# Kernel optimization log

Measured on AMD Instinct MI355X. Metric: run time of the kernel, lower is better.

## Reference

```python
import jax, jax.numpy as jnp
import numpy as np

HEADS = (4, 2, 1)
OUTS = (32, 16, 2)
NEG_SLOPE = 0.2


def gat_conv(x, src, dst, W, att_s, att_d, b, heads, out_dim, n_nodes, concat):
    # x: [N, Fin] -> h: [N, H, Fout]
    h = (x @ W).reshape(n_nodes, heads, out_dim)
    # per-node attention terms, gathered to edges: [E, H]
    a_src = jnp.sum(h * att_s, axis=-1)
    a_dst = jnp.sum(h * att_d, axis=-1)
    logits = jax.nn.leaky_relu(a_src[src] + a_dst[dst], NEG_SLOPE)
    # segment softmax over incoming edges of each destination node
    lmax = jax.ops.segment_max(logits, dst, num_segments=n_nodes)[dst]
    e = jnp.exp(logits - lmax)
    denom = jax.ops.segment_sum(e, dst, num_segments=n_nodes)[dst]
    alpha = e / denom  # [E, H]
    # weighted message aggregation
    msg = h[src] * alpha[:, :, None]  # [E, H, Fout]
    agg = jax.ops.segment_sum(msg, dst, num_segments=n_nodes)  # [N, H, Fout]
    if concat:
        agg = agg.reshape(n_nodes, heads * out_dim)
    else:
        agg = agg.mean(axis=1)
    return agg + b


def _glorot(key, shape):
    fan = shape[0] + shape[-1] if len(shape) == 2 else shape[-1] * 2
    s = jnp.sqrt(6.0 / fan)
    return jax.random.uniform(key, shape, jnp.float32, -s, s)


def setup_inputs() -> dict:
    key = jax.random.key(0)
    N, E, FIN = 100000, 1600000, 128
    ks = jax.random.split(key, 16)
    x = jax.random.normal(ks[0], (N, FIN), jnp.float32)
    edge_index = jax.random.randint(ks[1], (2, E), 0, N, jnp.int64)
    ins = (FIN, HEADS[0] * OUTS[0], HEADS[1] * OUTS[1])
    d = {"x": x, "edge_index": edge_index}
    for i in range(3):
        H, O = HEADS[i], OUTS[i]
        d[f"W{i+1}"] = _glorot(ks[2 + 4 * i], (ins[i], H * O))
        d[f"att_s{i+1}"] = _glorot(ks[3 + 4 * i], (H, O))
        d[f"att_d{i+1}"] = _glorot(ks[4 + 4 * i], (H, O))
        bdim = H * O if i < 2 else O
        d[f"b{i+1}"] = jnp.zeros((bdim,), jnp.float32)
    return d


def reference(x, edge_index, W1, att_s1, att_d1, b1, W2, att_s2, att_d2, b2, W3, att_s3, att_d3, b3):
    N = x.shape[0]
    loops = jnp.arange(N, dtype=edge_index.dtype)
    src = jnp.concatenate([edge_index[0], loops])
    dst = jnp.concatenate([edge_index[1], loops])
    h = gat_conv(x, src, dst, W1, att_s1, att_d1, b1, HEADS[0], OUTS[0], N, True)
    h = jax.nn.elu(h)
    h = gat_conv(h, src, dst, W2, att_s2, att_d2, b2, HEADS[1], OUTS[1], N, True)
    h = jax.nn.elu(h)
    h = gat_conv(h, src, dst, W3, att_s3, att_d3, b3, HEADS[2], OUTS[2], N, False)
    return jax.nn.log_softmax(h, axis=1)
```

## Files before the change

kernel.cpp:

```cpp
#include <hip/hip_runtime.h>
#include <math.h>

static __device__ __forceinline__ float lrelu(float x){ return fmaxf(x, 0.2f*x); }
static __device__ __forceinline__ float eluf(float x){ return x > 0.f ? x : __expf(x)-1.f; }
static __device__ __forceinline__ unsigned short f2bf(float f){
  unsigned int u = __float_as_uint(f);
  unsigned int r = (u + 0x7FFFu + ((u>>16)&1u)) >> 16;
  return (unsigned short)r;
}
static __device__ __forceinline__ float bflo(unsigned int u){ return __uint_as_float(u<<16); }
static __device__ __forceinline__ float bfhi(unsigned int u){ return __uint_as_float(u & 0xFFFF0000u); }

typedef __attribute__((ext_vector_type(8))) short short8;
typedef __attribute__((ext_vector_type(4))) float f32x4;

#define DETECT_IS64(ei_, s_is64_) \
  if (threadIdx.x < 64){ \
    int w_ = ((const int*)(ei_))[2*threadIdx.x + 1]; \
    unsigned long long b_ = __ballot(w_ != 0); \
    if (threadIdx.x == 0) s_is64_ = (b_ == 0ull); \
  } \
  __syncthreads();

__global__ void k_wprep(const float* __restrict__ W1, const float* __restrict__ W2,
                        unsigned short* __restrict__ wf1, unsigned short* __restrict__ wf2,
                        int* __restrict__ gbcnt, int* __restrict__ done, int NB){
  int e = blockIdx.x*256 + threadIdx.x;
  if (e < NB) gbcnt[e] = 0;
  if (e == 0) *done = 0;
  if (e < 2048){
    int lane = e&63, ct = (e>>6)&7, ks = e>>9;
    int q = lane>>4, n = lane&15;
    union { unsigned short us[8]; uint4 u; } pk;
    #pragma unroll
    for (int j=0;j<8;j++)
      pk.us[j] = f2bf(W1[(ks*32 + q*8 + j)*128 + ct*16 + n]);
    *(uint4*)&wf1[(size_t)e*8] = pk.u;
  } else if (e < 2048+512){
    int e2 = e - 2048;
    int lane = e2&63, ct = (e2>>6)&1, ks = e2>>7;
    int q = lane>>4, n = lane&15;
    union { unsigned short us[8]; uint4 u; } pk;
    #pragma unroll
    for (int j=0;j<8;j++)
      pk.us[j] = f2bf(W2[(ks*32 + q*8 + j)*32 + ct*16 + n]);
    *(uint4*)&wf2[(size_t)e2*8] = pk.u;
  }
}

__global__ __launch_bounds__(256) void k_bhist_scan(const void* __restrict__ ei,
    int* __restrict__ gbcnt, int* __restrict__ gbbase, int* __restrict__ gcursor,
    int* __restrict__ done, int E, int NB){
  extern __shared__ int lcnt[];
  __shared__ int s_is64;
  __shared__ int s_last;
  __shared__ int sh[256];
  __shared__ int carry;
  int t = threadIdx.x;
  for (int i=t; i<NB; i+=256) lcnt[i]=0;
  DETECT_IS64(ei, s_is64)
  int stride = gridDim.x*256;
  if (s_is64){
    const long long* p = (const long long*)ei;
    for (int e = blockIdx.x*256 + t; e < E; e += stride)
      atomicAdd(&lcnt[((int)p[(size_t)E+e])>>7], 1);
  } else {
    const int* p = (const int*)ei;
    for (int e = blockIdx.x*256 + t; e < E; e += stride)
      atomicAdd(&lcnt[p[(size_t)E+e]>>7], 1);
  }
  __syncthreads();
  for (int i=t; i<NB; i+=256){
    int c = lcnt[i];
    if (c) atomicAdd(&gbcnt[i], c);
  }
  __threadfence();
  if (t == 0){
    int old = atomicAdd(done, 1);
    s_last = (old == (int)gridDim.x - 1) ? 1 : 0;
  }
  __syncthreads();
  if (!s_last) return;
  if (t==0) carry = 0;
  __syncthreads();
  for (int base=0; base<NB; base+=256){
    int idx = base+t;
    int v = (idx<NB) ? atomicAdd(&gbcnt[idx], 0) : 0;
    sh[t]=v; __syncthreads();
    for (int off=1; off<256; off<<=1){
      int add = (t>=off)? sh[t-off] : 0;
      __syncthreads();
      sh[t]+=add;
      __syncthreads();
    }
    int excl = sh[t]-v+carry;
    if (idx<NB){ gbbase[idx]=excl; gcursor[idx]=excl; }
    __syncthreads();
    if (t==0) carry += sh[255];
    __syncthreads();
  }
}

#define BS_ITEMS 16
__global__ __launch_bounds__(256) void k_scat_gemm1(
    const void* __restrict__ ei, int* __restrict__ gcursor,
    unsigned int* __restrict__ ebuf, int E, int NB, int GS,
    const float* __restrict__ x, const unsigned short* __restrict__ wf,
    const float* __restrict__ atts, const float* __restrict__ attd,
    unsigned short* __restrict__ hb, float* __restrict__ as_, float* __restrict__ ad_,
    int N){
  __shared__ __align__(16) unsigned char smem[50176];
  __shared__ int s_is64;
  int t = threadIdx.x;
  if ((int)blockIdx.x < GS){
    int* lcnt  = (int*)smem;
    int* lbase = lcnt + NB;
    for (int i=t; i<NB; i+=256) lcnt[i]=0;
    DETECT_IS64(ei, s_is64)
    bool is64 = s_is64 != 0;
    int base = blockIdx.x*(256*BS_ITEMS);
    unsigned int ent[BS_ITEMS]; int bk[BS_ITEMS];
    #pragma unroll
    for (int i=0;i<BS_ITEMS;i++){
      int e = base + i*256 + t;
      if (e < E){
        int s, d;
        if (is64){ const long long* p=(const long long*)ei; s=(int)p[e]; d=(int)p[(size_t)E+e]; }
        else     { const int* p=(const int*)ei;            s=p[e];      d=p[(size_t)E+e]; }
        int b = d>>7;
        bk[i] = b;
        ent[i] = (unsigned int)s | ((unsigned int)(d & 127) << 25);
        atomicAdd(&lcnt[b], 1);
      } else bk[i] = -1;
    }
    __syncthreads();
    for (int i=t; i<NB; i+=256){
      int c = lcnt[i];
      lbase[i] = c ? atomicAdd(&gcursor[i], c) : 0;
    }
    __syncthreads();
    for (int i=t; i<NB; i+=256) lcnt[i]=0;
    __syncthreads();
    #pragma unroll
    for (int i=0;i<BS_ITEMS;i++){
      if (bk[i] >= 0){
        int pos = lbase[bk[i]] + atomicAdd(&lcnt[bk[i]], 1);
        ebuf[pos] = ent[i];
      }
    }
  } else {
    unsigned short* xs  = (unsigned short*)smem;
    unsigned short* wsm = (unsigned short*)(smem + 64*136*2);
    int r0 = ((int)blockIdx.x - GS)*64;
    {
      const uint4* src = (const uint4*)wf;
      uint4* dst = (uint4*)wsm;
      #pragma unroll
      for (int i=0;i<8;i++) dst[t + i*256] = src[t + i*256];
    }
    {
      #pragma unroll
      for (int i=0;i<4;i++){
        int idx = t + i*256;
        int row = idx>>4, k8 = (idx&15)*8;
        int gr = r0 + row;
        float4 v0 = make_float4(0.f,0.f,0.f,0.f), v1 = v0;
        if (gr < N){
          v0 = *(const float4*)&x[(size_t)gr*128 + k8];
          v1 = *(const float4*)&x[(size_t)gr*128 + k8 + 4];
        }
        union { unsigned short us[8]; uint4 u; } pk;
        pk.us[0]=f2bf(v0.x); pk.us[1]=f2bf(v0.y); pk.us[2]=f2bf(v0.z); pk.us[3]=f2bf(v0.w);
        pk.us[4]=f2bf(v1.x); pk.us[5]=f2bf(v1.y); pk.us[6]=f2bf(v1.z); pk.us[7]=f2bf(v1.w);
        *(uint4*)&xs[row*136 + k8] = pk.u;
      }
    }
    __syncthreads();
    int w = t>>6, lane = t&63, lm = lane&15, q = lane>>4;
    int rt0 = (w&1)*2;
    int ct0 = (w>>1)*4;
    f32x4 acc[2][4];
    #pragma unroll
    for (int a=0;a<2;a++)
      #pragma unroll
      for (int c=0;c<4;c++) acc[a][c] = (f32x4){0.f,0.f,0.f,0.f};
    #pragma unroll
    for (int ks=0;ks<4;ks++){
      short8 a0 = *(const short8*)&xs[( rt0   *16 + lm)*136 + ks*32 + q*8];
      short8 a1 = *(const short8*)&xs[((rt0+1)*16 + lm)*136 + ks*32 + q*8];
      #pragma unroll
      for (int c=0;c<4;c++){
        short8 b = *(const short8*)&wsm[((ks*8 + ct0 + c)*64 + lane)*8];
        acc[0][c] = __builtin_amdgcn_mfma_f32_16x16x32_bf16(a0, b, acc[0][c], 0,0,0);
        acc[1][c] = __builtin_amdgcn_mfma_f32_16x16x32_bf16(a1, b, acc[1][c], 0,0,0);
      }
    }
    __syncthreads();
    #pragma unroll
    for (int rl=0;rl<2;rl++)
      #pragma unroll
      for (int c=0;c<4;c++)
        #pragma unroll
        for (int r=0;r<4;r++)
          xs[((rt0+rl)*16 + q*4 + r)*136 + (ct0+c)*16 + lm] = f2bf(acc[rl][c][r]);
    __syncthreads();
    {
      #pragma unroll
      for (int i=0;i<4;i++){
        int idx = t + i*256;
        int row = idx>>4, c8 = (idx&15)*8;
        int gr = r0 + row;
        if (gr < N)
          *(uint4*)&hb[(size_t)gr*128 + c8] = *(const uint4*)&xs[row*136 + c8];
      }
    }
    {
      int row = t>>2, h = t&3;
      int gr = r0 + row;
      if (gr < N){
        const unsigned short* hr = &xs[row*136 + h*32];
        const float* sa = atts + h*32;
        const float* da = attd + h*32;
        float ss = 0.f, dd = 0.f;
        #pragma unroll
        for (int o=0;o<32;o+=8){
          uint4 v = *(const uint4*)&hr[o];
          float hv[8] = { bflo(v.x),bfhi(v.x),bflo(v.y),bfhi(v.y),
                          bflo(v.z),bfhi(v.z),bflo(v.w),bfhi(v.w) };
          #pragma unroll
          for (int m=0;m<8;m++){ ss += hv[m]*sa[o+m]; dd += hv[m]*da[o+m]; }
        }
        as_[gr*4+h] = ss; ad_[gr*4+h] = dd;
      }
    }
  }
}

__global__ __launch_bounds__(256) void k_bcsr(const unsigned int* __restrict__ ebuf,
    const int* __restrict__ gbbase, const int* __restrict__ gbcnt,
    int* __restrict__ rp, int* __restrict__ csr, int N, int NB, int E){
  __shared__ int lcnt[128];
  __shared__ int lexc[128];
  __shared__ int lcur[128];
  __shared__ int sc[256];
  int b = blockIdx.x, t = threadIdx.x;
  int d0 = b<<7;
  int R = N - d0; if (R > 128) R = 128;
  if (t < 128){ lcnt[t]=0; lcur[t]=0; }
  __syncthreads();
  int base = gbbase[b], cnt = gbcnt[b];
  for (int i=t; i<cnt; i+=256){
    unsigned int e = ebuf[base+i];
    atomicAdd(&lcnt[e>>25], 1);
  }
  __syncthreads();
  int v = (t<128)? lcnt[t] : 0;
  sc[t]=v; __syncthreads();
  for (int off=1; off<128; off<<=1){
    int add = (t>=off)? sc[t-off] : 0;
    __syncthreads();
    sc[t]+=add;
    __syncthreads();
  }
  if (t<128) lexc[t] = sc[t]-v;
  __syncthreads();
  if (t < R) rp[d0+t] = base + lexc[t];
  if (b == NB-1 && t == 0) rp[N] = E;
  for (int i=t; i<cnt; i+=256){
    unsigned int e = ebuf[base+i];
    int dl = e>>25;
    int pos = base + lexc[dl] + atomicAdd(&lcur[dl], 1);
    csr[pos] = (int)(e & 0x1FFFFFFu);
  }
}

__global__ __launch_bounds__(256) void k_mgemm2(const unsigned short* __restrict__ xb,
    const unsigned short* __restrict__ wf,
    const float* __restrict__ atts, const float* __restrict__ attd,
    unsigned short* __restrict__ hb2, float* __restrict__ as_, float* __restrict__ ad_,
    int N){
  __shared__ unsigned short xs[128*136];
  __shared__ unsigned short wsm[512*8];
  int t = threadIdx.x;
  int r0 = blockIdx.x*128;
  {
    #pragma unroll
    for (int i=0;i<2;i++)
      ((uint4*)wsm)[t + i*256] = ((const uint4*)wf)[t + i*256];
  }
  {
    #pragma unroll
    for (int i=0;i<8;i++){
      int idx = t + i*256;
      int row = idx>>4, c8 = (idx&15)*8;
      int gr = r0 + row;
      uint4 v = make_uint4(0u,0u,0u,0u);
      if (gr < N) v = *(const uint4*)&xb[(size_t)gr*128 + c8];
      *(uint4*)&xs[row*136 + c8] = v;
    }
  }
  __syncthreads();
  int w = t>>6, lane = t&63, lm = lane&15, q = lane>>4;
  int rt0 = 2*w;
  f32x4 acc[2][2];
  #pragma unroll
  for (int a=0;a<2;a++){ acc[a][0] = (f32x4){0.f,0.f,0.f,0.f}; acc[a][1] = acc[a][0]; }
  #pragma unroll
  for (int ks=0;ks<4;ks++){
    short8 a0 = *(const short8*)&xs[( rt0   *16 + lm)*136 + ks*32 + q*8];
    short8 a1 = *(const short8*)&xs[((rt0+1)*16 + lm)*136 + ks*32 + q*8];
    #pragma unroll
    for (int c=0;c<2;c++){
      short8 b = *(const short8*)&wsm[((ks*2 + c)*64 + lane)*8];
      acc[0][c] = __builtin_amdgcn_mfma_f32_16x16x32_bf16(a0, b, acc[0][c], 0,0,0);
      acc[1][c] = __builtin_amdgcn_mfma_f32_16x16x32_bf16(a1, b, acc[1][c], 0,0,0);
    }
  }
  __syncthreads();
  #pragma unroll
  for (int rl=0;rl<2;rl++)
    #pragma unroll
    for (int c=0;c<2;c++)
      #pragma unroll
      for (int r=0;r<4;r++)
        xs[((rt0+rl)*16 + q*4 + r)*136 + c*16 + lm] = f2bf(acc[rl][c][r]);
  __syncthreads();
  {
    #pragma unroll
    for (int i=0;i<2;i++){
      int idx = t + i*256;
      int row = idx>>2, c8 = (idx&3)*8;
      int gr = r0 + row;
      if (gr < N)
        *(uint4*)&hb2[(size_t)gr*32 + c8] = *(const uint4*)&xs[row*136 + c8];
    }
  }
  {
    int row = t>>1, h = t&1;
    int gr = r0 + row;
    if (gr < N){
      const unsigned short* hr = &xs[row*136 + h*16];
      const float* sa = atts + h*16;
      const float* da = attd + h*16;
      float ss = 0.f, dd = 0.f;
      #pragma unroll
      for (int o=0;o<16;o+=8){
        uint4 v = *(const uint4*)&hr[o];
        float hv[8] = { bflo(v.x),bfhi(v.x),bflo(v.y),bfhi(v.y),
                        bflo(v.z),bfhi(v.z),bflo(v.w),bfhi(v.w) };
        #pragma unroll
        for (int m=0;m<8;m++){ ss += hv[m]*sa[o+m]; dd += hv[m]*da[o+m]; }
      }
      as_[gr*2+h] = ss; ad_[gr*2+h] = dd;
    }
  }
}

__global__ __launch_bounds__(256) void k_agg1(const int* __restrict__ rp, const int* __restrict__ csr,
    const float* __restrict__ as_, const float* __restrict__ ad_,
    const uint4* __restrict__ hb4, const float* __restrict__ bias,
    unsigned short* __restrict__ outb, int N){
  int n = blockIdx.x*4 + (threadIdx.x>>6);
  if (n >= N) return;
  int lane = threadIdx.x & 63;
  int grp = lane>>4, li = lane&15, ghead = li>>2;
  int start = rp[n], end = rp[n+1];
  float adh = ad_[n*4+ghead];
  float l = 0.f;
  float a[8];
  #pragma unroll
  for (int k=0;k<8;k++) a[k]=0.f;
  if (grp == 0){
    float w = __expf(fminf(lrelu(as_[n*4+ghead] + adh), 80.f));
    l += w;
    uint4 v = hb4[(size_t)n*16 + li];
    a[0]+=w*bflo(v.x); a[1]+=w*bfhi(v.x); a[2]+=w*bflo(v.y); a[3]+=w*bfhi(v.y);
    a[4]+=w*bflo(v.z); a[5]+=w*bfhi(v.z); a[6]+=w*bflo(v.w); a[7]+=w*bfhi(v.w);
  }
  int i = start + grp;
  for (; i + 4 < end; i += 8){
    int s0 = csr[i];
    int s1 = csr[i+4];
    float w0 = __expf(fminf(lrelu(as_[s0*4+ghead] + adh), 80.f));
    float w1 = __expf(fminf(lrelu(as_[s1*4+ghead] + adh), 80.f));
    uint4 v0 = hb4[(size_t)s0*16 + li];
    uint4 v1 = hb4[(size_t)s1*16 + li];
    l += w0 + w1;
    a[0]+=w0*bflo(v0.x); a[1]+=w0*bfhi(v0.x); a[2]+=w0*bflo(v0.y); a[3]+=w0*bfhi(v0.y);
    a[4]+=w0*bflo(v0.z); a[5]+=w0*bfhi(v0.z); a[6]+=w0*bflo(v0.w); a[7]+=w0*bfhi(v0.w);
    a[0]+=w1*bflo(v1.x); a[1]+=w1*bfhi(v1.x); a[2]+=w1*bflo(v1.y); a[3]+=w1*bfhi(v1.y);
    a[4]+=w1*bflo(v1.z); a[5]+=w1*bfhi(v1.z); a[6]+=w1*bflo(v1.w); a[7]+=w1*bfhi(v1.w);
  }
  if (i < end){
    int s = csr[i];
    float w = __expf(fminf(lrelu(as_[s*4+ghead] + adh), 80.f));
    uint4 v = hb4[(size_t)s*16 + li];
    l += w;
    a[0]+=w*bflo(v.x); a[1]+=w*bfhi(v.x); a[2]+=w*bflo(v.y); a[3]+=w*bfhi(v.y);
    a[4]+=w*bflo(v.z); a[5]+=w*bfhi(v.z); a[6]+=w*bflo(v.w); a[7]+=w*bfhi(v.w);
  }
  l += __shfl_xor(l,1); l += __shfl_xor(l,2);
  l += __shfl_xor(l,16); l += __shfl_xor(l,32);
  #pragma unroll
  for (int msk=16; msk<64; msk<<=1){
    #pragma unroll
    for (int k=0;k<8;k++) a[k] += __shfl_xor(a[k], msk);
  }
  if (grp == 0){
    float invh = 4.f/l;
    float4 b0 = *(const float4*)&bias[li*8];
    float4 b1 = *(const float4*)&bias[li*8+4];
    union { unsigned short us[8]; uint4 v; } pk;
    pk.us[0]=f2bf(eluf(a[0]*invh+b0.x)); pk.us[1]=f2bf(eluf(a[1]*invh+b0.y));
    pk.us[2]=f2bf(eluf(a[2]*invh+b0.z)); pk.us[3]=f2bf(eluf(a[3]*invh+b0.w));
    pk.us[4]=f2bf(eluf(a[4]*invh+b1.x)); pk.us[5]=f2bf(eluf(a[5]*invh+b1.y));
    pk.us[6]=f2bf(eluf(a[6]*invh+b1.z)); pk.us[7]=f2bf(eluf(a[7]*invh+b1.w));
    *(uint4*)&outb[(size_t)n*128 + li*8] = pk.v;
  }
}

__global__ __launch_bounds__(256) void k_agg2(const int* __restrict__ rp, const int* __restrict__ csr,
    const float* __restrict__ as_, const float* __restrict__ ad_,
    const uint4* __restrict__ hb4, const float* __restrict__ bias,
    const float* __restrict__ W3, const float* __restrict__ atts3,
    const float* __restrict__ attd3,
    float4* __restrict__ pk4, int N){
  int n = blockIdx.x*4 + (threadIdx.x>>6);
  if (n >= N) return;
  int lane = threadIdx.x & 63;
  int grp = lane>>2, li = lane&3, ghead = li>>1;
  int start = rp[n], end = rp[n+1];
  float adh = ad_[n*2+ghead];
  float l = 0.f;
  float a[8];
  #pragma unroll
  for (int k=0;k<8;k++) a[k]=0.f;
  if (grp == 0){
    float w = __expf(fminf(lrelu(as_[n*2+ghead] + adh), 80.f));
    l += w;
    uint4 v = hb4[(size_t)n*4 + li];
    a[0]+=w*bflo(v.x); a[1]+=w*bfhi(v.x); a[2]+=w*bflo(v.y); a[3]+=w*bfhi(v.y);
    a[4]+=w*bflo(v.z); a[5]+=w*bfhi(v.z); a[6]+=w*bflo(v.w); a[7]+=w*bfhi(v.w);
  }
  int i = start + grp;
  for (; i + 16 < end; i += 32){
    int s0 = csr[i];
    int s1 = csr[i+16];
    float w0 = __expf(fminf(lrelu(as_[s0*2+ghead] + adh), 80.f));
    float w1 = __expf(fminf(lrelu(as_[s1*2+ghead] + adh), 80.f));
    uint4 v0 = hb4[(size_t)s0*4 + li];
    uint4 v1 = hb4[(size_t)s1*4 + li];
    l += w0 + w1;
    a[0]+=w0*bflo(v0.x); a[1]+=w0*bfhi(v0.x); a[2]+=w0*bflo(v0.y); a[3]+=w0*bfhi(v0.y);
    a[4]+=w0*bflo(v0.z); a[5]+=w0*bfhi(v0.z); a[6]+=w0*bflo(v0.w); a[7]+=w0*bfhi(v0.w);
    a[0]+=w1*bflo(v1.x); a[1]+=w1*bfhi(v1.x); a[2]+=w1*bflo(v1.y); a[3]+=w1*bfhi(v1.y);
    a[4]+=w1*bflo(v1.z); a[5]+=w1*bfhi(v1.z); a[6]+=w1*bflo(v1.w); a[7]+=w1*bfhi(v1.w);
  }
  if (i < end){
    int s = csr[i];
    float w = __expf(fminf(lrelu(as_[s*2+ghead] + adh), 80.f));
    uint4 v = hb4[(size_t)s*4 + li];
    l += w;
    a[0]+=w*bflo(v.x); a[1]+=w*bfhi(v.x); a[2]+=w*bflo(v.y); a[3]+=w*bfhi(v.y);
    a[4]+=w*bflo(v.z); a[5]+=w*bfhi(v.z); a[6]+=w*bflo(v.w); a[7]+=w*bfhi(v.w);
  }
  l += __shfl_xor(l,1);
  l += __shfl_xor(l,4); l += __shfl_xor(l,8);
  l += __shfl_xor(l,16); l += __shfl_xor(l,32);
  #pragma unroll
  for (int msk=4; msk<64; msk<<=1){
    #pragma unroll
    for (int k=0;k<8;k++) a[k] += __shfl_xor(a[k], msk);
  }
  float invh = 2.f/l;
  float r0_ = eluf(a[0]*invh + bias[li*8+0]);
  float r1_ = eluf(a[1]*invh + bias[li*8+1]);
  float r2_ = eluf(a[2]*invh + bias[li*8+2]);
  float r3_ = eluf(a[3]*invh + bias[li*8+3]);
  float r4_ = eluf(a[4]*invh + bias[li*8+4]);
  float r5_ = eluf(a[5]*invh + bias[li*8+5]);
  float r6_ = eluf(a[6]*invh + bias[li*8+6]);
  float r7_ = eluf(a[7]*invh + bias[li*8+7]);
  const float* wr = &W3[li*16];
  float p0 = r0_*wr[0] + r1_*wr[2] + r2_*wr[4]  + r3_*wr[6]
           + r4_*wr[8] + r5_*wr[10]+ r6_*wr[12] + r7_*wr[14];
  float p1 = r0_*wr[1] + r1_*wr[3] + r2_*wr[5]  + r3_*wr[7]
           + r4_*wr[9] + r5_*wr[11]+ r6_*wr[13] + r7_*wr[15];
  p0 += __shfl_xor(p0,1); p0 += __shfl_xor(p0,2);
  p1 += __shfl_xor(p1,1); p1 += __shfl_xor(p1,2);
  if (lane == 0){
    float4 pk;
    pk.x = p0; pk.y = p1;
    pk.z = p0*atts3[0] + p1*atts3[1];
    pk.w = p0*attd3[0] + p1*attd3[1];
    pk4[n] = pk;
  }
}

__global__ __launch_bounds__(256) void k_agg3(const int* __restrict__ rp, const int* __restrict__ csr,
    const float4* __restrict__ pk4, const float* __restrict__ bias,
    float* __restrict__ out, int N){
  int n = blockIdx.x*16 + (threadIdx.x>>4);
  if (n >= N) return;
  int li = threadIdx.x & 15;
  int start = rp[n], end = rp[n+1];
  float4 self = pk4[n];
  float adh = self.w;
  float l = 0.f;
  float2 acc = make_float2(0.f, 0.f);
  for (int i=start+li; i<end; i+=16){
    int s = csr[i];
    float4 ps = pk4[s];
    float w = __expf(fminf(lrelu(ps.z + adh), 80.f));
    l += w;
    acc.x += w*ps.x; acc.y += w*ps.y;
  }
  if (li == 0){
    float w = __expf(fminf(lrelu(self.z + adh), 80.f));
    l += w;
    acc.x += w*self.x; acc.y += w*self.y;
  }
  #pragma unroll
  for (int msk=1; msk<16; msk<<=1){
    l += __shfl_xor(l, msk);
    acc.x += __shfl_xor(acc.x, msk);
    acc.y += __shfl_xor(acc.y, msk);
  }
  if (li == 0){
    float inv = 1.f/l;
    float g0 = acc.x*inv + bias[0];
    float g1 = acc.y*inv + bias[1];
    float mm = fmaxf(g0, g1);
    float lse = mm + logf(__expf(g0-mm) + __expf(g1-mm));
    *(float2*)&out[2*n] = make_float2(g0-lse, g1-lse);
  }
}

extern "C" void kernel_launch(void* const* d_in, const int* in_sizes, int n_in,
                              void* d_out, int out_size, void* d_ws, size_t ws_size,
                              hipStream_t stream) {
  const float* x   = (const float*)d_in[0];
  const void*  ei  = d_in[1];
  const float* W1  = (const float*)d_in[2];
  const float* as1 = (const float*)d_in[3];
  const float* ad1 = (const float*)d_in[4];
  const float* b1  = (const float*)d_in[5];
  const float* W2  = (const float*)d_in[6];
  const float* as2 = (const float*)d_in[7];
  const float* ad2 = (const float*)d_in[8];
  const float* b2  = (const float*)d_in[9];
  const float* W3  = (const float*)d_in[10];
  const float* as3 = (const float*)d_in[11];
  const float* ad3 = (const float*)d_in[12];
  const float* b3  = (const float*)d_in[13];

  int N = in_sizes[0] / 128;
  int E = in_sizes[1] / 2;
  int NB = (N + 127) >> 7;

  char* w = (char*)d_ws;
  size_t off = 0;
  auto alloc = [&](size_t bytes)->void*{
    void* p = w + off; off += (bytes + 255) & ~(size_t)255; return p;
  };
  int*   gbcnt   = (int*)alloc((size_t)NB*4);
  int*   gbbase  = (int*)alloc((size_t)NB*4);
  int*   gcursor = (int*)alloc((size_t)NB*4);
  int*   done    = (int*)alloc(256);
  int*   rp      = (int*)alloc((size_t)(N+1)*4);
  unsigned int* ebuf = (unsigned int*)alloc((size_t)E*4);
  int*   csr     = (int*)alloc((size_t)E*4);
  float* as_buf  = (float*)alloc((size_t)N*4*4);
  float* ad_buf  = (float*)alloc((size_t)N*4*4);
  unsigned short* wf1 = (unsigned short*)alloc(2048*8*2);
  unsigned short* wf2 = (unsigned short*)alloc(512*8*2);
  unsigned short* hb  = (unsigned short*)alloc((size_t)N*128*2);
  unsigned short* xb  = (unsigned short*)alloc((size_t)N*128*2);
  unsigned short* hb2 = (unsigned short*)alloc((size_t)N*32*2);
  float4* pk4    = (float4*)alloc((size_t)N*16);
  if (off > ws_size) return;

  k_wprep<<<10, 256, 0, stream>>>(W1, W2, wf1, wf2, gbcnt, done, NB);
  k_bhist_scan<<<256, 256, NB*4, stream>>>(ei, gbcnt, gbbase, gcursor, done, E, NB);

  int GS = (E + 256*BS_ITEMS - 1) / (256*BS_ITEMS);
  int G1 = (N + 63)/64;
  k_scat_gemm1<<<GS + G1, 256, 0, stream>>>(ei, gcursor, ebuf, E, NB, GS,
                                            x, wf1, as1, ad1, hb, as_buf, ad_buf, N);
  k_bcsr<<<NB, 256, 0, stream>>>(ebuf, gbbase, gbcnt, rp, csr, N, NB, E);

  k_agg1<<<(N + 3)/4, 256, 0, stream>>>(rp, csr, as_buf, ad_buf, (const uint4*)hb, b1, xb, N);

  k_mgemm2<<<(N + 127)/128, 256, 0, stream>>>(xb, wf2, as2, ad2, hb2, as_buf, ad_buf, N);
  k_agg2<<<(N + 3)/4, 256, 0, stream>>>(rp, csr, as_buf, ad_buf, (const uint4*)hb2, b2,
                                        W3, as3, ad3, pk4, N);

  k_agg3<<<(N + 15)/16, 256, 0, stream>>>(rp, csr, pk4, b3, (float*)d_out, N);
}
```

Before: 338.3 us.

## Assign one node per lane-group in aggregation, drop edge-split shuffles, use exp2

k_agg1 and k_agg2 previously spread each node's edges across 4 or 16 sub-groups of a wave and then combined them with cross-lane shuffles. They now give each node only its feature-width lanes (16 or 4) and loop over all of that node's edges serially, so the shuffle reduction goes away and more nodes fit per block. Attention logits are pre-scaled by log2(e) so the kernels can call the hardware exp2 directly. Gather offsets use 32-bit byte arithmetic. The trade-off is less memory-level parallelism per node: with about 17 edges per node, each lane group now runs a longer serial gather chain.

Result: faster. 317.0 us (-6.3%).

```diff
diff --git a/kernel.cpp b/kernel.cpp
--- a/kernel.cpp
+++ b/kernel.cpp
@@ -3,6 +3,7 @@
 
 static __device__ __forceinline__ float lrelu(float x){ return fmaxf(x, 0.2f*x); }
 static __device__ __forceinline__ float eluf(float x){ return x > 0.f ? x : __expf(x)-1.f; }
+static __device__ __forceinline__ float fexp2(float x){ return __builtin_amdgcn_exp2f(x); }
 static __device__ __forceinline__ unsigned short f2bf(float f){
   unsigned int u = __float_as_uint(f);
   unsigned int r = (u + 0x7FFFu + ((u>>16)&1u)) >> 16;
@@ -11,8 +12,18 @@
 static __device__ __forceinline__ float bflo(unsigned int u){ return __uint_as_float(u<<16); }
 static __device__ __forceinline__ float bfhi(unsigned int u){ return __uint_as_float(u & 0xFFFF0000u); }
 
+#define LOG2E 1.44269504f
+#define CLAMP2 115.41f
+
 typedef __attribute__((ext_vector_type(8))) short short8;
 typedef __attribute__((ext_vector_type(4))) float f32x4;
+
+static __device__ __forceinline__ uint4 ld16(const uint4* base, unsigned eoff){
+  return *(const uint4*)((const char*)base + (size_t)(eoff*16u));
+}
+static __device__ __forceinline__ float ldf(const float* base, unsigned eoff){
+  return *(const float*)((const char*)base + (size_t)(eoff*4u));
+}
 
 #define DETECT_IS64(ei_, s_is64_) \
   if (threadIdx.x < 64){ \
@@ -230,7 +241,7 @@
           #pragma unroll
           for (int m=0;m<8;m++){ ss += hv[m]*sa[o+m]; dd += hv[m]*da[o+m]; }
         }
-        as_[gr*4+h] = ss; ad_[gr*4+h] = dd;
+        as_[gr*4+h] = ss*LOG2E; ad_[gr*4+h] = dd*LOG2E;
       }
     }
   }
@@ -351,72 +362,58 @@
         #pragma unroll
         for (int m=0;m<8;m++){ ss += hv[m]*sa[o+m]; dd += hv[m]*da[o+m]; }
       }
-      as_[gr*2+h] = ss; ad_[gr*2+h] = dd;
-    }
-  }
-}
+      as_[gr*2+h] = ss*LOG2E; ad_[gr*2+h] = dd*LOG2E;
+    }
+  }
+}
+
+#define ACC8(v_, w_) { \
+  a[0]+=w_*bflo(v_.x); a[1]+=w_*bfhi(v_.x); a[2]+=w_*bflo(v_.y); a[3]+=w_*bfhi(v_.y); \
+  a[4]+=w_*bflo(v_.z); a[5]+=w_*bfhi(v_.z); a[6]+=w_*bflo(v_.w); a[7]+=w_*bfhi(v_.w); }
 
 __global__ __launch_bounds__(256) void k_agg1(const int* __restrict__ rp, const int* __restrict__ csr,
     const float* __restrict__ as_, const float* __restrict__ ad_,
     const uint4* __restrict__ hb4, const float* __restrict__ bias,
     unsigned short* __restrict__ outb, int N){
-  int n = blockIdx.x*4 + (threadIdx.x>>6);
+  int n = blockIdx.x*16 + (threadIdx.x>>4);
   if (n >= N) return;
-  int lane = threadIdx.x & 63;
-  int grp = lane>>4, li = lane&15, ghead = li>>2;
+  int li = threadIdx.x & 15, ghead = li>>2;
   int start = rp[n], end = rp[n+1];
-  float adh = ad_[n*4+ghead];
-  float l = 0.f;
+  float adh = ldf(ad_, (unsigned)n*4u+ghead);
   float a[8];
   #pragma unroll
   for (int k=0;k<8;k++) a[k]=0.f;
-  if (grp == 0){
-    float w = __expf(fminf(lrelu(as_[n*4+ghead] + adh), 80.f));
-    l += w;
-    uint4 v = hb4[(size_t)n*16 + li];
-    a[0]+=w*bflo(v.x); a[1]+=w*bfhi(v.x); a[2]+=w*bflo(v.y); a[3]+=w*bfhi(v.y);
-    a[4]+=w*bflo(v.z); a[5]+=w*bfhi(v.z); a[6]+=w*bflo(v.w); a[7]+=w*bfhi(v.w);
-  }
-  int i = start + grp;
-  for (; i + 4 < end; i += 8){
+  float wse = fexp2(fminf(lrelu(ldf(as_, (unsigned)n*4u+ghead) + adh), CLAMP2));
+  float l = wse;
+  { uint4 v = ld16(hb4, (unsigned)n*16u + li); ACC8(v, wse) }
+  int i = start;
+  for (; i + 1 < end; i += 2){
     int s0 = csr[i];
-    int s1 = csr[i+4];
-    float w0 = __expf(fminf(lrelu(as_[s0*4+ghead] + adh), 80.f));
-    float w1 = __expf(fminf(lrelu(as_[s1*4+ghead] + adh), 80.f));
-    uint4 v0 = hb4[(size_t)s0*16 + li];
-    uint4 v1 = hb4[(size_t)s1*16 + li];
+    int s1 = csr[i+1];
+    float w0 = fexp2(fminf(lrelu(ldf(as_, (unsigned)s0*4u+ghead) + adh), CLAMP2));
+    float w1 = fexp2(fminf(lrelu(ldf(as_, (unsigned)s1*4u+ghead) + adh), CLAMP2));
+    uint4 v0 = ld16(hb4, (unsigned)s0*16u + li);
+    uint4 v1 = ld16(hb4, (unsigned)s1*16u + li);
     l += w0 + w1;
-    a[0]+=w0*bflo(v0.x); a[1]+=w0*bfhi(v0.x); a[2]+=w0*bflo(v0.y); a[3]+=w0*bfhi(v0.y);
-    a[4]+=w0*bflo(v0.z); a[5]+=w0*bfhi(v0.z); a[6]+=w0*bflo(v0.w); a[7]+=w0*bfhi(v0.w);
-    a[0]+=w1*bflo(v1.x); a[1]+=w1*bfhi(v1.x); a[2]+=w1*bflo(v1.y); a[3]+=w1*bfhi(v1.y);
-    a[4]+=w1*bflo(v1.z); a[5]+=w1*bfhi(v1.z); a[6]+=w1*bflo(v1.w); a[7]+=w1*bfhi(v1.w);
+    ACC8(v0, w0)
+    ACC8(v1, w1)
   }
   if (i < end){
     int s = csr[i];
-    float w = __expf(fminf(lrelu(as_[s*4+ghead] + adh), 80.f));
-    uint4 v = hb4[(size_t)s*16 + li];
+    float w = fexp2(fminf(lrelu(ldf(as_, (unsigned)s*4u+ghead) + adh), CLAMP2));
+    uint4 v = ld16(hb4, (unsigned)s*16u + li);
     l += w;
-    a[0]+=w*bflo(v.x); a[1]+=w*bfhi(v.x); a[2]+=w*bflo(v.y); a[3]+=w*bfhi(v.y);
-    a[4]+=w*bflo(v.z); a[5]+=w*bfhi(v.z); a[6]+=w*bflo(v.w); a[7]+=w*bfhi(v.w);
-  }
-  l += __shfl_xor(l,1); l += __shfl_xor(l,2);
-  l += __shfl_xor(l,16); l += __shfl_xor(l,32);
-  #pragma unroll
-  for (int msk=16; msk<64; msk<<=1){
-    #pragma unroll
-    for (int k=0;k<8;k++) a[k] += __shfl_xor(a[k], msk);
-  }
-  if (grp == 0){
-    float invh = 4.f/l;
-    float4 b0 = *(const float4*)&bias[li*8];
-    float4 b1 = *(const float4*)&bias[li*8+4];
-    union { unsigned short us[8]; uint4 v; } pk;
-    pk.us[0]=f2bf(eluf(a[0]*invh+b0.x)); pk.us[1]=f2bf(eluf(a[1]*invh+b0.y));
-    pk.us[2]=f2bf(eluf(a[2]*invh+b0.z)); pk.us[3]=f2bf(eluf(a[3]*invh+b0.w));
-    pk.us[4]=f2bf(eluf(a[4]*invh+b1.x)); pk.us[5]=f2bf(eluf(a[5]*invh+b1.y));
-    pk.us[6]=f2bf(eluf(a[6]*invh+b1.z)); pk.us[7]=f2bf(eluf(a[7]*invh+b1.w));
-    *(uint4*)&outb[(size_t)n*128 + li*8] = pk.v;
-  }
+    ACC8(v, w)
+  }
+  float invh = 1.f/l;
+  float4 b0 = *(const float4*)&bias[li*8];
+  float4 b1 = *(const float4*)&bias[li*8+4];
+  union { unsigned short us[8]; uint4 v; } pk;
+  pk.us[0]=f2bf(eluf(a[0]*invh+b0.x)); pk.us[1]=f2bf(eluf(a[1]*invh+b0.y));
+  pk.us[2]=f2bf(eluf(a[2]*invh+b0.z)); pk.us[3]=f2bf(eluf(a[3]*invh+b0.w));
+  pk.us[4]=f2bf(eluf(a[4]*invh+b1.x)); pk.us[5]=f2bf(eluf(a[5]*invh+b1.y));
+  pk.us[6]=f2bf(eluf(a[6]*invh+b1.z)); pk.us[7]=f2bf(eluf(a[7]*invh+b1.w));
+  *(uint4*)&outb[(size_t)n*128 + li*8] = pk.v;
 }
 
 __global__ __launch_bounds__(256) void k_agg2(const int* __restrict__ rp, const int* __restrict__ csr,
@@ -425,54 +422,37 @@
     const float* __restrict__ W3, const float* __restrict__ atts3,
     const float* __restrict__ attd3,
     float4* __restrict__ pk4, int N){
-  int n = blockIdx.x*4 + (threadIdx.x>>6);
+  int n = blockIdx.x*64 + (threadIdx.x>>2);
   if (n >= N) return;
-  int lane = threadIdx.x & 63;
-  int grp = lane>>2, li = lane&3, ghead = li>>1;
+  int li = threadIdx.x & 3, ghead = li>>1;
   int start = rp[n], end = rp[n+1];
-  float adh = ad_[n*2+ghead];
-  float l = 0.f;
+  float adh = ldf(ad_, (unsigned)n*2u+ghead);
   float a[8];
   #pragma unroll
   for (int k=0;k<8;k++) a[k]=0.f;
-  if (grp == 0){
-    float w = __expf(fminf(lrelu(as_[n*2+ghead] + adh), 80.f));
-    l += w;
-    uint4 v = hb4[(size_t)n*4 + li];
-    a[0]+=w*bflo(v.x); a[1]+=w*bfhi(v.x); a[2]+=w*bflo(v.y); a[3]+=w*bfhi(v.y);
-    a[4]+=w*bflo(v.z); a[5]+=w*bfhi(v.z); a[6]+=w*bflo(v.w); a[7]+=w*bfhi(v.w);
-  }
-  int i = start + grp;
-  for (; i + 16 < end; i += 32){
+  float wse = fexp2(fminf(lrelu(ldf(as_, (unsigned)n*2u+ghead) + adh), CLAMP2));
+  float l = wse;
+  { uint4 v = ld16(hb4, (unsigned)n*4u + li); ACC8(v, wse) }
+  int i = start;
+  for (; i + 1 < end; i += 2){
     int s0 = csr[i];
-    int s1 = csr[i+16];
-    float w0 = __expf(fminf(lrelu(as_[s0*2+ghead] + adh), 80.f));
-    float w1 = __expf(fminf(lrelu(as_[s1*2+ghead] + adh), 80.f));
-    uint4 v0 = hb4[(size_t)s0*4 + li];
-    uint4 v1 = hb4[(size_t)s1*4 + li];
+    int s1 = csr[i+1];
+    float w0 = fexp2(fminf(lrelu(ldf(as_, (unsigned)s0*2u+ghead) + adh), CLAMP2));
+    float w1 = fexp2(fminf(lrelu(ldf(as_, (unsigned)s1*2u+ghead) + adh), CLAMP2));
+    uint4 v0 = ld16(hb4, (unsigned)s0*4u + li);
+    uint4 v1 = ld16(hb4, (unsigned)s1*4u + li);
     l += w0 + w1;
-    a[0]+=w0*bflo(v0.x); a[1]+=w0*bfhi(v0.x); a[2]+=w0*bflo(v0.y); a[3]+=w0*bfhi(v0.y);
-    a[4]+=w0*bflo(v0.z); a[5]+=w0*bfhi(v0.z); a[6]+=w0*bflo(v0.w); a[7]+=w0*bfhi(v0.w);
-    a[0]+=w1*bflo(v1.x); a[1]+=w1*bfhi(v1.x); a[2]+=w1*bflo(v1.y); a[3]+=w1*bfhi(v1.y);
-    a[4]+=w1*bflo(v1.z); a[5]+=w1*bfhi(v1.z); a[6]+=w1*bflo(v1.w); a[7]+=w1*bfhi(v1.w);
+    ACC8(v0, w0)
+    ACC8(v1, w1)
   }
   if (i < end){
     int s = csr[i];
-    float w = __expf(fminf(lrelu(as_[s*2+ghead] + adh), 80.f));
-    uint4 v = hb4[(size_t)s*4 + li];
+    float w = fexp2(fminf(lrelu(ldf(as_, (unsigned)s*2u+ghead) + adh), CLAMP2));
+    uint4 v = ld16(hb4, (unsigned)s*4u + li);
     l += w;
-    a[0]+=w*bflo(v.x); a[1]+=w*bfhi(v.x); a[2]+=w*bflo(v.y); a[3]+=w*bfhi(v.y);
-    a[4]+=w*bflo(v.z); a[5]+=w*bfhi(v.z); a[6]+=w*bflo(v.w); a[7]+=w*bfhi(v.w);
-  }
-  l += __shfl_xor(l,1);
-  l += __shfl_xor(l,4); l += __shfl_xor(l,8);
-  l += __shfl_xor(l,16); l += __shfl_xor(l,32);
-  #pragma unroll
-  for (int msk=4; msk<64; msk<<=1){
-    #pragma unroll
-    for (int k=0;k<8;k++) a[k] += __shfl_xor(a[k], msk);
-  }
-  float invh = 2.f/l;
+    ACC8(v, w)
+  }
+  float invh = 1.f/l;
   float r0_ = eluf(a[0]*invh + bias[li*8+0]);
   float r1_ = eluf(a[1]*invh + bias[li*8+1]);
   float r2_ = eluf(a[2]*invh + bias[li*8+2]);
@@ -488,11 +468,11 @@
            + r4_*wr[9] + r5_*wr[11]+ r6_*wr[13] + r7_*wr[15];
   p0 += __shfl_xor(p0,1); p0 += __shfl_xor(p0,2);
   p1 += __shfl_xor(p1,1); p1 += __shfl_xor(p1,2);
-  if (lane == 0){
+  if (li == 0){
     float4 pk;
     pk.x = p0; pk.y = p1;
-    pk.z = p0*atts3[0] + p1*atts3[1];
-    pk.w = p0*attd3[0] + p1*attd3[1];
+    pk.z = (p0*atts3[0] + p1*atts3[1])*LOG2E;
+    pk.w = (p0*attd3[0] + p1*attd3[1])*LOG2E;
     pk4[n] = pk;
   }
 }
@@ -511,12 +491,12 @@
   for (int i=start+li; i<end; i+=16){
     int s = csr[i];
     float4 ps = pk4[s];
-    float w = __expf(fminf(lrelu(ps.z + adh), 80.f));
+    float w = fexp2(fminf(lrelu(ps.z + adh), CLAMP2));
     l += w;
     acc.x += w*ps.x; acc.y += w*ps.y;
   }
   if (li == 0){
-    float w = __expf(fminf(lrelu(self.z + adh), 80.f));
+    float w = fexp2(fminf(lrelu(self.z + adh), CLAMP2));
     l += w;
     acc.x += w*self.x; acc.y += w*self.y;
   }
@@ -589,11 +569,11 @@
                                             x, wf1, as1, ad1, hb, as_buf, ad_buf, N);
   k_bcsr<<<NB, 256, 0, stream>>>(ebuf, gbbase, gbcnt, rp, csr, N, NB, E);
 
-  k_agg1<<<(N + 3)/4, 256, 0, stream>>>(rp, csr, as_buf, ad_buf, (const uint4*)hb, b1, xb, N);
+  k_agg1<<<(N + 15)/16, 256, 0, stream>>>(rp, csr, as_buf, ad_buf, (const uint4*)hb, b1, xb, N);
 
   k_mgemm2<<<(N + 127)/128, 256, 0, stream>>>(xb, wf2, as2, ad2, hb2, as_buf, ad_buf, N);
-  k_agg2<<<(N + 3)/4, 256, 0, stream>>>(rp, csr, as_buf, ad_buf, (const uint4*)hb2, b2,
-                                        W3, as3, ad3, pk4, N);
+  k_agg2<<<(N + 63)/64, 256, 0, stream>>>(rp, csr, as_buf, ad_buf, (const uint4*)hb2, b2,
+                                          W3, as3, ad3, pk4, N);
 
   k_agg3<<<(N + 15)/16, 256, 0, stream>>>(rp, csr, pk4, b3, (float*)d_out, N);
 }
```
